# Kernel optimization log

Measured on AMD Instinct MI355X. Metric: run time of the kernel, lower is better.

## Reference

```python
import jax, jax.numpy as jnp
import numpy as np

EPS = 1e-5
HEADS = 8


def _bn(x, p):
    # p: [4, C] rows = (gamma, beta, running_mean, running_var); channel axis = 1 (eval-mode BN)
    shape = (1, p.shape[1]) + (1,) * (x.ndim - 2)
    g = p[0].reshape(shape); b = p[1].reshape(shape)
    m = p[2].reshape(shape); v = p[3].reshape(shape)
    return (x - m) * (g / jnp.sqrt(v + EPS)) + b


def _conv1x1(x, w):
    # x: [N, Cin, H, W], w: [Cout, Cin]
    return jnp.einsum('oc,nchw->nohw', w, x)


def _axial(x, kqv_w, kqv_bn, logits_bn, rel_enc, ks, height_dim):
    # x: [B, C, H, W]
    if height_dim:
        x = jnp.transpose(x, (0, 3, 1, 2))  # [B, W, C, H] -> attend over H (=ks)
    else:
        x = jnp.transpose(x, (0, 2, 1, 3))  # [B, H, C, W] -> attend over W (=ks)
    b, w, d, h = x.shape
    dh = d // HEADS
    xf = x.reshape(b * w, d, h)
    kqv = jnp.einsum('oc,ncl->nol', kqv_w, xf)          # conv1d k=1, [n, 2d, h]
    kqv = _bn(kqv, kqv_bn)
    kqv = kqv.reshape(b * w, HEADS, dh * 2, h)
    k = kqv[:, :, : dh // 2]                            # [n, H, dh/2, h]
    q = kqv[:, :, dh // 2: dh]                          # [n, H, dh/2, h]
    v = kqv[:, :, dh:]                                  # [n, H, dh,   h]
    # relative position encodings
    idx = jnp.arange(ks)[None, :] - jnp.arange(ks)[:, None] + ks - 1  # [ks, ks]
    rel = rel_enc[:, idx.reshape(-1)].reshape(dh * 2, ks, ks)
    q_enc = rel[: dh // 2]
    k_enc = rel[dh // 2: dh]
    v_enc = rel[dh:]
    qk = jnp.einsum('nhdx,nhdy->nhxy', q, k)
    qr = jnp.einsum('nhdx,dxy->nhxy', q, q_enc)
    kr = jnp.einsum('nhdx,dxy->nhyx', k, k_enc)         # einsum + transpose(2,3)
    logits = jnp.concatenate([qk, qr, kr], axis=1)       # [n, 3*H, h, h]
    logits = _bn(logits, logits_bn)
    logits = logits.reshape(b * w, 3, HEADS, h, h).sum(axis=1)
    weights = jax.nn.softmax(logits, axis=3)             # [n, H, h, h]
    attn = jnp.einsum('nhxy,nhdy->nhdx', weights, v)
    attn_enc = jnp.einsum('nhxy,dxy->nhdx', weights, v_enc)
    # cat along last dim + reshape + sum(dim=-2) in torch == elementwise sum here
    out = (attn + attn_enc).reshape(b, w, d, h)
    if height_dim:
        out = jnp.transpose(out, (0, 2, 3, 1))  # [B, C, H, W]
    else:
        out = jnp.transpose(out, (0, 2, 1, 3))  # [B, C, H, W]
    return out


def setup_inputs() -> dict:
    key = jax.random.key(0)
    ks = jax.random.split(key, 13)
    def rn(k, shape, s=0.05):
        return jax.random.normal(k, shape, jnp.float32) * s
    def rp(k, shape):
        return jax.random.uniform(k, shape, jnp.float32, minval=0.1, maxval=1.0)
    return {
        'x': jax.random.normal(ks[0], (1, 64, 256, 128), jnp.float32),
        'conv1_w': rn(ks[1], (64, 64)),
        'bn1': rp(ks[2], (4, 64)),
        'kqv_w_h': rn(ks[3], (128, 64)),
        'kqv_bn_h': rp(ks[4], (4, 128)),
        'logits_bn_h': rp(ks[5], (4, 24)),
        'rel_enc_h': rn(ks[6], (16, 511)),
        'kqv_w_w': rn(ks[7], (128, 64)),
        'kqv_bn_w': rp(ks[8], (4, 128)),
        'logits_bn_w': rp(ks[9], (4, 24)),
        'rel_enc_w': rn(ks[10], (16, 255)),
        'conv3_w': rn(ks[11], (64, 64)),
        'bn3': rp(ks[12], (4, 64)),
    }


def reference(x, conv1_w, bn1, kqv_w_h, kqv_bn_h, logits_bn_h, rel_enc_h,
              kqv_w_w, kqv_bn_w, logits_bn_w, rel_enc_w, conv3_w, bn3):
    out = jax.nn.relu(_bn(_conv1x1(x, conv1_w), bn1))
    out = _axial(out, kqv_w_h, kqv_bn_h, logits_bn_h, rel_enc_h, 256, True)
    out = _axial(out, kqv_w_w, kqv_bn_w, logits_bn_w, rel_enc_w, 128, False)
    out = jax.nn.relu(out)
    out = _bn(_conv1x1(out, conv3_w), bn3)
    return jax.nn.relu(out + x)
```

## Files before the change

kernel.cpp:

```cpp
#include <hip/hip_runtime.h>
#include <stdint.h>

#define EPSF 1e-5f
#define LOG2E 1.4426950408889634f

typedef float f32x2 __attribute__((ext_vector_type(2)));
typedef float f32x4 __attribute__((ext_vector_type(4)));

__device__ __forceinline__ float bflo(uint32_t u){ union{uint32_t u;float f;}c; c.u=u<<16; return c.f; }
__device__ __forceinline__ float bfhi(uint32_t u){ union{uint32_t u;float f;}c; c.u=u&0xffff0000u; return c.f; }
__device__ __forceinline__ float bfhiraw(uint32_t u){ union{uint32_t u;float f;}c; c.u=u; return c.f; }
__device__ __forceinline__ uint32_t f2bf(float f){ union{float f;uint32_t u;}c; c.f=f; uint32_t u=c.u; return (u + 0x7fffu + ((u>>16)&1u)) >> 16; }
__device__ __forceinline__ uint32_t pk2(float a, float b){ return f2bf(a) | (f2bf(b)<<16); }

__device__ __forceinline__ f32x2 pk_add(f32x2 a, f32x2 b){
  f32x2 d; asm("v_pk_add_f32 %0, %1, %2" : "=v"(d) : "v"(a), "v"(b)); return d;
}
__device__ __forceinline__ f32x2 pk_mul(f32x2 a, f32x2 b){
  f32x2 d; asm("v_pk_mul_f32 %0, %1, %2" : "=v"(d) : "v"(a), "v"(b)); return d;
}
__device__ __forceinline__ f32x2 pk_fma(f32x2 a, f32x2 b, f32x2 c){
  f32x2 d; asm("v_pk_fma_f32 %0, %1, %2, %3" : "=v"(d) : "v"(a), "v"(b), "v"(c)); return d;
}
__device__ __forceinline__ f32x2 up2(uint32_t u){
  f32x2 r; r.x = bflo(u); r.y = bfhiraw(u); return r;
}

__global__ void k_relpack(const float* __restrict__ relH, const float* __restrict__ relW,
                          uint4* __restrict__ rqkH, uint4* __restrict__ rveH,
                          uint4* __restrict__ rqkW, uint4* __restrict__ rveW) {
  int NJ = blockIdx.x ? 255 : 511;
  const float* rel = blockIdx.x ? relW : relH;
  uint4* rqk = blockIdx.x ? rqkW : rqkH;
  uint4* rve = blockIdx.x ? rveW : rveH;
  int j = threadIdx.x;
  if (j >= NJ) return;
  const float* q = rel;
  const float* k = rel + 4*NJ;
  const float* v = rel + 8*NJ;
  int jr = NJ-1-j;
  uint4 a;
  a.x = pk2(q[0*NJ+j], q[1*NJ+j]);
  a.y = pk2(q[2*NJ+j], q[3*NJ+j]);
  a.z = pk2(k[0*NJ+jr], k[1*NJ+jr]);
  a.w = pk2(k[2*NJ+jr], k[3*NJ+jr]);
  rqk[j] = a;
  uint4 b;
  b.x = pk2(v[0*NJ+j], v[1*NJ+j]);
  b.y = pk2(v[2*NJ+j], v[3*NJ+j]);
  b.z = pk2(v[4*NJ+j], v[5*NJ+j]);
  b.w = pk2(v[6*NJ+j], v[7*NJ+j]);
  rve[j] = b;
}

__global__ __launch_bounds__(256)
void k_conv1(const float* __restrict__ in, const float* __restrict__ w,
             const float* __restrict__ bn, float* __restrict__ out) {
  __shared__ float L[64*65];
  int tid = threadIdx.x;
  int p0 = blockIdx.x * 64;
  int lane = tid & 63;
  int wvs = __builtin_amdgcn_readfirstlane(tid >> 6);
  #pragma unroll
  for (int rr = 0; rr < 16; ++rr) {
    int c = wvs*16 + rr;
    L[lane*65 + c] = in[(size_t)c*32768 + p0 + lane];
  }
  __syncthreads();
  f32x2 xv2[32];
  #pragma unroll
  for (int c2 = 0; c2 < 32; ++c2) {
    xv2[c2].x = L[lane*65 + 2*c2];
    xv2[c2].y = L[lane*65 + 2*c2 + 1];
  }
  float val[16];
  #pragma unroll
  for (int r = 0; r < 16; ++r) {
    int o = wvs*16 + r;
    const f32x2* wr = (const f32x2*)(w + o*64);
    f32x2 a2 = {0.f, 0.f};
    #pragma unroll
    for (int c2 = 0; c2 < 32; ++c2) a2 = wr[c2]*xv2[c2] + a2;
    float acc = a2.x + a2.y;
    float s = bn[o] * rsqrtf(bn[192+o] + EPSF);
    val[r] = fmaxf(fmaf(acc, s, fmaf(-bn[128+o], s, bn[64+o])), 0.f);
  }
  __syncthreads();
  #pragma unroll
  for (int r = 0; r < 16; ++r) L[lane*65 + wvs*16 + r] = val[r];
  __syncthreads();
  float4* dst = (float4*)(out + (size_t)p0*64);
  #pragma unroll
  for (int k = 0; k < 4; ++k) {
    int f4 = tid + k*256;
    int f = f4*4; int p = f >> 6, o = f & 63;
    float4 v;
    v.x = L[p*65+o]; v.y = L[p*65+o+1]; v.z = L[p*65+o+2]; v.w = L[p*65+o+3];
    dst[f4] = v;
  }
}

template<int LEN, int RS, int CS>
__global__ __launch_bounds__(512)
void k_kqv(const float* __restrict__ in, const float* __restrict__ w,
           const float* __restrict__ bn, uint4* __restrict__ kvV,
           uint2* __restrict__ kvK, float* __restrict__ qb) {
  __shared__ float L[64*65];
  int tid = threadIdx.x;
  int n = blockIdx.x;
  int y0 = blockIdx.y * 64;
  #pragma unroll
  for (int rr = 0; rr < 8; ++rr) {
    int idx = tid + rr*512;
    int yy = idx >> 6, c = idx & 63;
    L[yy*65 + c] = in[((size_t)(y0+yy)*RS + (size_t)n*CS)*64 + c];
  }
  __syncthreads();
  int hd = __builtin_amdgcn_readfirstlane(tid >> 6);
  int yy = tid & 63;
  f32x2 xv2[32];
  #pragma unroll
  for (int c2 = 0; c2 < 32; ++c2) {
    xv2[c2].x = L[yy*65 + 2*c2];
    xv2[c2].y = L[yy*65 + 2*c2 + 1];
  }
  float val[16];
  #pragma unroll
  for (int r = 0; r < 16; ++r) {
    int o = hd*16 + r;
    const f32x2* wr = (const f32x2*)(w + o*64);
    f32x2 a2 = {0.f, 0.f};
    #pragma unroll
    for (int c2 = 0; c2 < 32; ++c2) a2 = wr[c2]*xv2[c2] + a2;
    float acc = a2.x + a2.y;
    float s = bn[o] * rsqrtf(bn[384+o] + EPSF);
    val[r] = fmaf(acc, s, fmaf(-bn[256+o], s, bn[128+o]));
  }
  size_t base = ((size_t)n*8 + hd)*LEN + (y0 + yy);
  kvK[base] = make_uint2(pk2(val[0],val[1]), pk2(val[2],val[3]));
  kvV[base] = make_uint4(pk2(val[8],val[9]),  pk2(val[10],val[11]),
                         pk2(val[12],val[13]), pk2(val[14],val[15]));
  float4 qq; qq.x = val[4]; qq.y = val[5]; qq.z = val[6]; qq.w = val[7];
  *(float4*)(qb + base*4) = qq;
}

struct E4 { f32x2 qe0, qe1, ke0, ke1; };
struct V4 { f32x2 a, b, c, d; };

__device__ __forceinline__ E4 upQK(uint4 u){
  E4 r; r.qe0 = up2(u.x); r.qe1 = up2(u.y); r.ke0 = up2(u.z); r.ke1 = up2(u.w); return r;
}
__device__ __forceinline__ V4 upVE(uint4 u){
  V4 r; r.a = up2(u.x); r.b = up2(u.y); r.c = up2(u.z); r.d = up2(u.w); return r;
}
__device__ __forceinline__ float pairA(f32x2 q01, f32x2 q23, const E4& e,
                                       f32x2 ktlo, f32x2 kthi) {
  f32x2 t0 = pk_add(q01, e.ke0);
  f32x2 t1 = pk_add(q23, e.ke1);
  f32x2 s  = pk_mul(t0, ktlo);
  s = pk_fma(t1, kthi, s);
  s = pk_fma(q01, e.qe0, s);
  s = pk_fma(q23, e.qe1, s);
  return s.x + s.y;
}
__device__ __forceinline__ void pairB(float ex, const V4& ve,
                                      f32x2 va01, f32x2 va23, f32x2 vb01, f32x2 vb23,
                                      f32x2* A, float& ss) {
  ss += ex;
  f32x2 e2; e2.x = ex; e2.y = ex;
  A[0] = pk_fma(e2, pk_add(va01, ve.a), A[0]);
  A[1] = pk_fma(e2, pk_add(va23, ve.b), A[1]);
  A[2] = pk_fma(e2, pk_add(vb01, ve.c), A[2]);
  A[3] = pk_fma(e2, pk_add(vb23, ve.d), A[3]);
}

template<int LEN, int G, bool RELUO, int XS, int NS>
__global__ __launch_bounds__(LEN/4*G, 2)
void k_attn5(const uint4* __restrict__ kvV, const uint2* __restrict__ kvK,
             const float* __restrict__ qb, const uint4* __restrict__ rqk,
             const uint4* __restrict__ rve, const float* __restrict__ lbn,
             float* __restrict__ out) {
  constexpr int NJ = 2*LEN-1;
  constexpr int NJ4 = (NJ+1)/4;
  constexpr int XT = LEN/4;
  constexpr int T = XT*G;
  constexpr int YR = LEN/G;
  constexpr size_t S1 = (size_t)LEN*48 + (size_t)NJ4*4*16*2;
  constexpr size_t S2 = (size_t)(G-1)*LEN*40;
  constexpr size_t PS = S1 > S2 ? S1 : S2;
  int n  = blockIdx.x >> 3;
  int hd = blockIdx.x & 7;
  int t  = threadIdx.x;

  __shared__ __align__(16) char pool[PS];
  f32x4* sKt = (f32x4*)(pool);
  f32x4* sVa = (f32x4*)(pool + (size_t)LEN*16);
  f32x4* sVb = (f32x4*)(pool + (size_t)LEN*32);
  uint4* tQK = (uint4*)(pool + (size_t)LEN*48);
  uint4* tVE = (uint4*)(pool + (size_t)LEN*48 + (size_t)NJ4*64);

  float A0L, A1L, A2L;
  {
    int c0 = hd, c1 = 8+hd, c2 = 16+hd;
    A0L = lbn[c0]*rsqrtf(lbn[72+c0]+EPSF)*LOG2E;
    A1L = lbn[c1]*rsqrtf(lbn[72+c1]+EPSF)*LOG2E;
    A2L = lbn[c2]*rsqrtf(lbn[72+c2]+EPSF)*LOG2E;
  }
  float A0g = (fabsf(A0L) > 1e-25f) ? A0L : copysignf(1e-25f, A0L);
  float ratio = A2L / A0g;

  size_t kvbase = ((size_t)n*8 + hd)*LEN;
  for (int i = t; i < LEN; i += T) {
    uint2 kk = kvK[kvbase + i];
    uint4 vv = kvV[kvbase + i];
    f32x4 kt; kt.x=bflo(kk.x)*A0g; kt.y=bfhi(kk.x)*A0g; kt.z=bflo(kk.y)*A0g; kt.w=bfhi(kk.y)*A0g;
    sKt[i] = kt;
    f32x4 va; va.x=bflo(vv.x); va.y=bfhi(vv.x); va.z=bflo(vv.y); va.w=bfhi(vv.y);
    sVa[i] = va;
    f32x4 vb; vb.x=bflo(vv.z); vb.y=bfhi(vv.z); vb.z=bflo(vv.w); vb.w=bfhi(vv.w);
    sVb[i] = vb;
  }
  for (int j = t; j < NJ; j += T) {
    uint4 a = rqk[j];
    uint4 sq;
    sq.x = pk2(bflo(a.x)*A1L,   bfhi(a.x)*A1L);
    sq.y = pk2(bflo(a.y)*A1L,   bfhi(a.y)*A1L);
    sq.z = pk2(bflo(a.z)*ratio, bfhi(a.z)*ratio);
    sq.w = pk2(bflo(a.w)*ratio, bfhi(a.w)*ratio);
    int r = j & 3, mm = j >> 2;
    tQK[r*NJ4 + mm] = sq;
    tVE[r*NJ4 + mm] = rve[j];
  }

  int g  = t / XT;
  int tl = t % XT;
  int y0 = g * YR;
  int x0 = 4 * tl;

  f32x2 q01[4], q23[4];
  #pragma unroll
  for (int i = 0; i < 4; ++i) {
    f32x4 qq = *(const f32x4*)(qb + (kvbase + x0 + i)*4);
    q01[i].x = qq.x; q01[i].y = qq.y;
    q23[i].x = qq.z; q23[i].y = qq.w;
  }

  float m[4], ss[4];
  f32x2 acc[4][4];
  #pragma unroll
  for (int i=0;i<4;++i){ m[i]=-3.0e38f; ss[i]=0.f;
    #pragma unroll
    for(int d=0;d<4;++d){ acc[i][d].x=0.f; acc[i][d].y=0.f; } }

  __syncthreads();

  int mi = ((y0 + LEN-1) >> 2) - tl;
  E4 Wq0 = upQK(tQK[0*NJ4 + mi]), Wq1 = upQK(tQK[1*NJ4 + mi]), Wq2 = upQK(tQK[2*NJ4 + mi]);
  V4 Wv0 = upVE(tVE[0*NJ4 + mi]), Wv1 = upVE(tVE[1*NJ4 + mi]), Wv2 = upVE(tVE[2*NJ4 + mi]);

  for (int cc = 0; cc < YR/4; ++cc) {
    int yb = y0 + 4*cc;
    int ma = mi + cc;
    int mb = ma + 1;
    float lr[4][4];
    E4 E3 = upQK(tQK[3*NJ4 + ma]);
    { f32x4 kt = sKt[yb]; f32x2 kl = kt.lo, kh = kt.hi;
      lr[0][0]=pairA(q01[0],q23[0],E3, kl,kh); lr[1][0]=pairA(q01[1],q23[1],Wq2,kl,kh);
      lr[2][0]=pairA(q01[2],q23[2],Wq1,kl,kh); lr[3][0]=pairA(q01[3],q23[3],Wq0,kl,kh); }
    E4 E0 = upQK(tQK[0*NJ4 + mb]);
    { f32x4 kt = sKt[yb+1]; f32x2 kl = kt.lo, kh = kt.hi;
      lr[0][1]=pairA(q01[0],q23[0],E0, kl,kh); lr[1][1]=pairA(q01[1],q23[1],E3, kl,kh);
      lr[2][1]=pairA(q01[2],q23[2],Wq2,kl,kh); lr[3][1]=pairA(q01[3],q23[3],Wq1,kl,kh); }
    E4 E1 = upQK(tQK[1*NJ4 + mb]);
    { f32x4 kt = sKt[yb+2]; f32x2 kl = kt.lo, kh = kt.hi;
      lr[0][2]=pairA(q01[0],q23[0],E1, kl,kh); lr[1][2]=pairA(q01[1],q23[1],E0, kl,kh);
      lr[2][2]=pairA(q01[2],q23[2],E3, kl,kh); lr[3][2]=pairA(q01[3],q23[3],Wq2,kl,kh); }
    E4 E2 = upQK(tQK[2*NJ4 + mb]);
    { f32x4 kt = sKt[yb+3]; f32x2 kl = kt.lo, kh = kt.hi;
      lr[0][3]=pairA(q01[0],q23[0],E2, kl,kh); lr[1][3]=pairA(q01[1],q23[1],E1, kl,kh);
      lr[2][3]=pairA(q01[2],q23[2],E0, kl,kh); lr[3][3]=pairA(q01[3],q23[3],E3, kl,kh); }
    Wq0 = E0; Wq1 = E1; Wq2 = E2;
    #pragma unroll
    for (int i = 0; i < 4; ++i) {
      float cm = fmaxf(fmaxf(lr[i][0], lr[i][1]), fmaxf(lr[i][2], lr[i][3]));
      float mn = fmaxf(m[i], cm);
      float sc = __builtin_amdgcn_exp2f(m[i] - mn);
      m[i] = mn; ss[i] *= sc;
      f32x2 sc2; sc2.x = sc; sc2.y = sc;
      #pragma unroll
      for (int d = 0; d < 4; ++d) acc[i][d] = pk_mul(acc[i][d], sc2);
    }
    V4 F3 = upVE(tVE[3*NJ4 + ma]);
    { f32x4 va = sVa[yb], vb = sVb[yb];
      pairB(__builtin_amdgcn_exp2f(lr[0][0]-m[0]), F3,  va.lo,va.hi,vb.lo,vb.hi, acc[0], ss[0]);
      pairB(__builtin_amdgcn_exp2f(lr[1][0]-m[1]), Wv2, va.lo,va.hi,vb.lo,vb.hi, acc[1], ss[1]);
      pairB(__builtin_amdgcn_exp2f(lr[2][0]-m[2]), Wv1, va.lo,va.hi,vb.lo,vb.hi, acc[2], ss[2]);
      pairB(__builtin_amdgcn_exp2f(lr[3][0]-m[3]), Wv0, va.lo,va.hi,vb.lo,vb.hi, acc[3], ss[3]); }
    V4 F0 = upVE(tVE[0*NJ4 + mb]);
    { f32x4 va = sVa[yb+1], vb = sVb[yb+1];
      pairB(__builtin_amdgcn_exp2f(lr[0][1]-m[0]), F0,  va.lo,va.hi,vb.lo,vb.hi, acc[0], ss[0]);
      pairB(__builtin_amdgcn_exp2f(lr[1][1]-m[1]), F3,  va.lo,va.hi,vb.lo,vb.hi, acc[1], ss[1]);
      pairB(__builtin_amdgcn_exp2f(lr[2][1]-m[2]), Wv2, va.lo,va.hi,vb.lo,vb.hi, acc[2], ss[2]);
      pairB(__builtin_amdgcn_exp2f(lr[3][1]-m[3]), Wv1, va.lo,va.hi,vb.lo,vb.hi, acc[3], ss[3]); }
    V4 F1 = upVE(tVE[1*NJ4 + mb]);
    { f32x4 va = sVa[yb+2], vb = sVb[yb+2];
      pairB(__builtin_amdgcn_exp2f(lr[0][2]-m[0]), F1,  va.lo,va.hi,vb.lo,vb.hi, acc[0], ss[0]);
      pairB(__builtin_amdgcn_exp2f(lr[1][2]-m[1]), F0,  va.lo,va.hi,vb.lo,vb.hi, acc[1], ss[1]);
      pairB(__builtin_amdgcn_exp2f(lr[2][2]-m[2]), F3,  va.lo,va.hi,vb.lo,vb.hi, acc[2], ss[2]);
      pairB(__builtin_amdgcn_exp2f(lr[3][2]-m[3]), Wv2, va.lo,va.hi,vb.lo,vb.hi, acc[3], ss[3]); }
    V4 F2 = upVE(tVE[2*NJ4 + mb]);
    { f32x4 va = sVa[yb+3], vb = sVb[yb+3];
      pairB(__builtin_amdgcn_exp2f(lr[0][3]-m[0]), F2,  va.lo,va.hi,vb.lo,vb.hi, acc[0], ss[0]);
      pairB(__builtin_amdgcn_exp2f(lr[1][3]-m[1]), F1,  va.lo,va.hi,vb.lo,vb.hi, acc[1], ss[1]);
      pairB(__builtin_amdgcn_exp2f(lr[2][3]-m[2]), F0,  va.lo,va.hi,vb.lo,vb.hi, acc[2], ss[2]);
      pairB(__builtin_amdgcn_exp2f(lr[3][3]-m[3]), F3,  va.lo,va.hi,vb.lo,vb.hi, acc[3], ss[3]); }
    Wv0 = F0; Wv1 = F1; Wv2 = F2;
  }

  __syncthreads();
  float4* M0 = (float4*)(pool);
  float4* M1 = (float4*)(pool + (size_t)(G-1)*LEN*16);
  float2* MS = (float2*)(pool + (size_t)(G-1)*LEN*32);
  if (g > 0) {
    #pragma unroll
    for (int i = 0; i < 4; ++i) {
      int slot = (g-1)*LEN + x0 + i;
      M0[slot] = make_float4(acc[i][0].x,acc[i][0].y,acc[i][1].x,acc[i][1].y);
      M1[slot] = make_float4(acc[i][2].x,acc[i][2].y,acc[i][3].x,acc[i][3].y);
      MS[slot] = make_float2(m[i], ss[i]);
    }
  }
  __syncthreads();
  if (g == 0) {
    #pragma unroll
    for (int i = 0; i < 4; ++i) {
      float M = m[i];
      float2 oms[G-1];
      #pragma unroll
      for (int gg = 1; gg < G; ++gg) {
        oms[gg-1] = MS[(gg-1)*LEN + x0 + i];
        M = fmaxf(M, oms[gg-1].x);
      }
      float w0 = __builtin_amdgcn_exp2f(m[i] - M);
      float st = ss[i]*w0;
      float a[8];
      a[0]=acc[i][0].x*w0; a[1]=acc[i][0].y*w0; a[2]=acc[i][1].x*w0; a[3]=acc[i][1].y*w0;
      a[4]=acc[i][2].x*w0; a[5]=acc[i][2].y*w0; a[6]=acc[i][3].x*w0; a[7]=acc[i][3].y*w0;
      #pragma unroll
      for (int gg = 1; gg < G; ++gg) {
        int slot = (gg-1)*LEN + x0 + i;
        float wg = __builtin_amdgcn_exp2f(oms[gg-1].x - M);
        st += oms[gg-1].y*wg;
        float4 a0 = M0[slot];
        float4 a1 = M1[slot];
        a[0] = fmaf(a0.x, wg, a[0]); a[1] = fmaf(a0.y, wg, a[1]);
        a[2] = fmaf(a0.z, wg, a[2]); a[3] = fmaf(a0.w, wg, a[3]);
        a[4] = fmaf(a1.x, wg, a[4]); a[5] = fmaf(a1.y, wg, a[5]);
        a[6] = fmaf(a1.z, wg, a[6]); a[7] = fmaf(a1.w, wg, a[7]);
      }
      float inv = 1.0f / st;
      float* dst = out + ((size_t)(x0+i)*XS + (size_t)n*NS)*64 + hd*8;
      float4 lo, hi;
      lo.x = a[0]*inv; lo.y = a[1]*inv; lo.z = a[2]*inv; lo.w = a[3]*inv;
      hi.x = a[4]*inv; hi.y = a[5]*inv; hi.z = a[6]*inv; hi.w = a[7]*inv;
      if (RELUO) {
        lo.x=fmaxf(lo.x,0.f); lo.y=fmaxf(lo.y,0.f); lo.z=fmaxf(lo.z,0.f); lo.w=fmaxf(lo.w,0.f);
        hi.x=fmaxf(hi.x,0.f); hi.y=fmaxf(hi.y,0.f); hi.z=fmaxf(hi.z,0.f); hi.w=fmaxf(hi.w,0.f);
      }
      *(float4*)dst = lo;
      *((float4*)dst + 1) = hi;
    }
  }
}

__global__ __launch_bounds__(256)
void k_conv3(const float* __restrict__ in, const float* __restrict__ w,
             const float* __restrict__ bn, const float* __restrict__ resid,
             float* __restrict__ out) {
  __shared__ float L[64*65];
  int tid = threadIdx.x;
  int p0 = blockIdx.x * 64;
  const float4* src = (const float4*)(in + (size_t)p0*64);
  #pragma unroll
  for (int k = 0; k < 4; ++k) {
    int f4 = tid + k*256;
    float4 v = src[f4];
    int f = f4*4; int p = f >> 6, o = f & 63;
    L[p*65+o] = v.x; L[p*65+o+1] = v.y; L[p*65+o+2] = v.z; L[p*65+o+3] = v.w;
  }
  __syncthreads();
  int lane = tid & 63;
  int wvs = __builtin_amdgcn_readfirstlane(tid >> 6);
  f32x2 xv2[32];
  #pragma unroll
  for (int c2 = 0; c2 < 32; ++c2) {
    xv2[c2].x = L[lane*65 + 2*c2];
    xv2[c2].y = L[lane*65 + 2*c2 + 1];
  }
  #pragma unroll
  for (int r = 0; r < 16; ++r) {
    int o = wvs*16 + r;
    const f32x2* wr = (const f32x2*)(w + o*64);
    f32x2 a2 = {0.f, 0.f};
    #pragma unroll
    for (int c2 = 0; c2 < 32; ++c2) a2 = wr[c2]*xv2[c2] + a2;
    float acc = a2.x + a2.y;
    float s = bn[o] * rsqrtf(bn[192+o] + EPSF);
    float val = fmaf(acc, s, fmaf(-bn[128+o], s, bn[64+o]));
    size_t idx = (size_t)o*32768 + p0 + lane;
    out[idx] = fmaxf(val + resid[idx], 0.f);
  }
}

extern "C" void kernel_launch(void* const* d_in, const int* in_sizes, int n_in,
                              void* d_out, int out_size, void* d_ws, size_t ws_size,
                              hipStream_t stream) {
  const float* x         = (const float*)d_in[0];
  const float* conv1_w   = (const float*)d_in[1];
  const float* bn1       = (const float*)d_in[2];
  const float* kqv_w_h   = (const float*)d_in[3];
  const float* kqv_bn_h  = (const float*)d_in[4];
  const float* lbn_h     = (const float*)d_in[5];
  const float* rel_h     = (const float*)d_in[6];
  const float* kqv_w_w   = (const float*)d_in[7];
  const float* kqv_bn_w  = (const float*)d_in[8];
  const float* lbn_w     = (const float*)d_in[9];
  const float* rel_w     = (const float*)d_in[10];
  const float* conv3_w   = (const float*)d_in[11];
  const float* bn3       = (const float*)d_in[12];
  float* outp = (float*)d_out;
  char* ws = (char*)d_ws;

  float* A    = (float*)(ws);
  uint4* kvV  = (uint4*)(ws + 8388608);
  uint2* kvK  = (uint2*)(ws + 12582912);
  float* qb   = (float*)(ws + 14680064);
  uint4* rqkH = (uint4*)(ws + 18874368);
  uint4* rveH = (uint4*)(ws + 18882560);
  uint4* rqkW = (uint4*)(ws + 18890752);
  uint4* rveW = (uint4*)(ws + 18894848);

  k_relpack<<<2, 512, 0, stream>>>(rel_h, rel_w, rqkH, rveH, rqkW, rveW);

  k_conv1<<<512, 256, 0, stream>>>(x, conv1_w, bn1, A);

  k_kqv<256,128,1><<<dim3(128,4), 512, 0, stream>>>(A, kqv_w_h, kqv_bn_h, kvV, kvK, qb);
  k_attn5<256,4,false,128,1><<<1024, 256, 0, stream>>>(kvV, kvK, qb, rqkH, rveH, lbn_h, A);

  k_kqv<128,1,128><<<dim3(256,2), 512, 0, stream>>>(A, kqv_w_w, kqv_bn_w, kvV, kvK, qb);
  k_attn5<128,4,true,1,128><<<2048, 128, 0, stream>>>(kvV, kvK, qb, rqkW, rveW, lbn_w, A);

  k_conv3<<<512, 256, 0, stream>>>(A, conv3_w, bn3, x, outp);
}
```

Before: 178.3 us.

## Split attention query rows across blocks and use more key groups with serial merge

The attention kernel gains a query-row tile parameter, so the height pass now splits each (n, head) into two blocks of 128 query rows, and both passes use 8 key groups instead of 4. The cross-group softmax merge becomes a sequential pairwise reduction through a small shared buffer sized for one group, with barriers per step. This is meant to raise the number of waves in flight and shorten each thread's key loop. In exchange, each block loads the full K/V and relative tables again, and the merge adds extra synchronisation rounds.

```diff
diff --git a/kernel.cpp b/kernel.cpp
--- a/kernel.cpp
+++ b/kernel.cpp
@@ -174,22 +174,26 @@
   A[3] = pk_fma(e2, pk_add(vb23, ve.d), A[3]);
 }
 
-template<int LEN, int G, bool RELUO, int XS, int NS>
-__global__ __launch_bounds__(LEN/4*G, 2)
-void k_attn5(const uint4* __restrict__ kvV, const uint2* __restrict__ kvK,
+template<int LEN, int XR, int G, bool RELUO, int XS, int NS>
+__global__ __launch_bounds__(XR/4*G, 2)
+void k_attn6(const uint4* __restrict__ kvV, const uint2* __restrict__ kvK,
              const float* __restrict__ qb, const uint4* __restrict__ rqk,
              const uint4* __restrict__ rve, const float* __restrict__ lbn,
              float* __restrict__ out) {
   constexpr int NJ = 2*LEN-1;
   constexpr int NJ4 = (NJ+1)/4;
-  constexpr int XT = LEN/4;
+  constexpr int XT = XR/4;
   constexpr int T = XT*G;
   constexpr int YR = LEN/G;
+  constexpr int NXB = LEN/XR;
   constexpr size_t S1 = (size_t)LEN*48 + (size_t)NJ4*4*16*2;
-  constexpr size_t S2 = (size_t)(G-1)*LEN*40;
+  constexpr size_t S2 = (size_t)XR*40;
   constexpr size_t PS = S1 > S2 ? S1 : S2;
-  int n  = blockIdx.x >> 3;
-  int hd = blockIdx.x & 7;
+  int bx = blockIdx.x;
+  int xh = bx % NXB;
+  int nh = bx / NXB;
+  int n  = nh >> 3;
+  int hd = nh & 7;
   int t  = threadIdx.x;
 
   __shared__ __align__(16) char pool[PS];
@@ -235,7 +239,7 @@
   int g  = t / XT;
   int tl = t % XT;
   int y0 = g * YR;
-  int x0 = 4 * tl;
+  int x0 = xh*XR + 4*tl;
 
   f32x2 q01[4], q23[4];
   #pragma unroll
@@ -254,7 +258,7 @@
 
   __syncthreads();
 
-  int mi = ((y0 + LEN-1) >> 2) - tl;
+  int mi = ((y0 + LEN-1) >> 2) - (x0 >> 2);
   E4 Wq0 = upQK(tQK[0*NJ4 + mi]), Wq1 = upQK(tQK[1*NJ4 + mi]), Wq2 = upQK(tQK[2*NJ4 + mi]);
   V4 Wv0 = upVE(tVE[0*NJ4 + mi]), Wv1 = upVE(tVE[1*NJ4 + mi]), Wv2 = upVE(tVE[2*NJ4 + mi]);
 
@@ -319,50 +323,54 @@
 
   __syncthreads();
   float4* M0 = (float4*)(pool);
-  float4* M1 = (float4*)(pool + (size_t)(G-1)*LEN*16);
-  float2* MS = (float2*)(pool + (size_t)(G-1)*LEN*32);
-  if (g > 0) {
+  float4* M1 = (float4*)(pool + (size_t)XR*16);
+  float2* MS = (float2*)(pool + (size_t)XR*32);
+  int xl = 4*tl;
+  for (int gg = 1; gg < G; ++gg) {
+    if (g == gg) {
+      #pragma unroll
+      for (int i = 0; i < 4; ++i) {
+        M0[xl+i] = make_float4(acc[i][0].x,acc[i][0].y,acc[i][1].x,acc[i][1].y);
+        M1[xl+i] = make_float4(acc[i][2].x,acc[i][2].y,acc[i][3].x,acc[i][3].y);
+        MS[xl+i] = make_float2(m[i], ss[i]);
+      }
+    }
+    __syncthreads();
+    if (g == 0) {
+      #pragma unroll
+      for (int i = 0; i < 4; ++i) {
+        float2 os = MS[xl+i];
+        float M = fmaxf(m[i], os.x);
+        float w0 = __builtin_amdgcn_exp2f(m[i] - M);
+        float wg = __builtin_amdgcn_exp2f(os.x - M);
+        m[i] = M;
+        ss[i] = ss[i]*w0 + os.y*wg;
+        float4 a0 = M0[xl+i];
+        float4 a1 = M1[xl+i];
+        f32x2 w02; w02.x=w0; w02.y=w0;
+        f32x2 wg2; wg2.x=wg; wg2.y=wg;
+        f32x2 b0; b0.x=a0.x; b0.y=a0.y;
+        f32x2 b1; b1.x=a0.z; b1.y=a0.w;
+        f32x2 b2; b2.x=a1.x; b2.y=a1.y;
+        f32x2 b3; b3.x=a1.z; b3.y=a1.w;
+        acc[i][0] = pk_fma(acc[i][0], w02, pk_mul(b0, wg2));
+        acc[i][1] = pk_fma(acc[i][1], w02, pk_mul(b1, wg2));
+        acc[i][2] = pk_fma(acc[i][2], w02, pk_mul(b2, wg2));
+        acc[i][3] = pk_fma(acc[i][3], w02, pk_mul(b3, wg2));
+      }
+    }
+    __syncthreads();
+  }
+  if (g == 0) {
     #pragma unroll
     for (int i = 0; i < 4; ++i) {
-      int slot = (g-1)*LEN + x0 + i;
-      M0[slot] = make_float4(acc[i][0].x,acc[i][0].y,acc[i][1].x,acc[i][1].y);
-      M1[slot] = make_float4(acc[i][2].x,acc[i][2].y,acc[i][3].x,acc[i][3].y);
-      MS[slot] = make_float2(m[i], ss[i]);
-    }
-  }
-  __syncthreads();
-  if (g == 0) {
-    #pragma unroll
-    for (int i = 0; i < 4; ++i) {
-      float M = m[i];
-      float2 oms[G-1];
-      #pragma unroll
-      for (int gg = 1; gg < G; ++gg) {
-        oms[gg-1] = MS[(gg-1)*LEN + x0 + i];
-        M = fmaxf(M, oms[gg-1].x);
-      }
-      float w0 = __builtin_amdgcn_exp2f(m[i] - M);
-      float st = ss[i]*w0;
-      float a[8];
-      a[0]=acc[i][0].x*w0; a[1]=acc[i][0].y*w0; a[2]=acc[i][1].x*w0; a[3]=acc[i][1].y*w0;
-      a[4]=acc[i][2].x*w0; a[5]=acc[i][2].y*w0; a[6]=acc[i][3].x*w0; a[7]=acc[i][3].y*w0;
-      #pragma unroll
-      for (int gg = 1; gg < G; ++gg) {
-        int slot = (gg-1)*LEN + x0 + i;
-        float wg = __builtin_amdgcn_exp2f(oms[gg-1].x - M);
-        st += oms[gg-1].y*wg;
-        float4 a0 = M0[slot];
-        float4 a1 = M1[slot];
-        a[0] = fmaf(a0.x, wg, a[0]); a[1] = fmaf(a0.y, wg, a[1]);
-        a[2] = fmaf(a0.z, wg, a[2]); a[3] = fmaf(a0.w, wg, a[3]);
-        a[4] = fmaf(a1.x, wg, a[4]); a[5] = fmaf(a1.y, wg, a[5]);
-        a[6] = fmaf(a1.z, wg, a[6]); a[7] = fmaf(a1.w, wg, a[7]);
-      }
-      float inv = 1.0f / st;
+      float inv = 1.0f / ss[i];
       float* dst = out + ((size_t)(x0+i)*XS + (size_t)n*NS)*64 + hd*8;
       float4 lo, hi;
-      lo.x = a[0]*inv; lo.y = a[1]*inv; lo.z = a[2]*inv; lo.w = a[3]*inv;
-      hi.x = a[4]*inv; hi.y = a[5]*inv; hi.z = a[6]*inv; hi.w = a[7]*inv;
+      lo.x = acc[i][0].x*inv; lo.y = acc[i][0].y*inv;
+      lo.z = acc[i][1].x*inv; lo.w = acc[i][1].y*inv;
+      hi.x = acc[i][2].x*inv; hi.y = acc[i][2].y*inv;
+      hi.z = acc[i][3].x*inv; hi.w = acc[i][3].y*inv;
       if (RELUO) {
         lo.x=fmaxf(lo.x,0.f); lo.y=fmaxf(lo.y,0.f); lo.z=fmaxf(lo.z,0.f); lo.w=fmaxf(lo.w,0.f);
         hi.x=fmaxf(hi.x,0.f); hi.y=fmaxf(hi.y,0.f); hi.z=fmaxf(hi.z,0.f); hi.w=fmaxf(hi.w,0.f);
@@ -445,10 +453,10 @@
   k_conv1<<<512, 256, 0, stream>>>(x, conv1_w, bn1, A);
 
   k_kqv<256,128,1><<<dim3(128,4), 512, 0, stream>>>(A, kqv_w_h, kqv_bn_h, kvV, kvK, qb);
-  k_attn5<256,4,false,128,1><<<1024, 256, 0, stream>>>(kvV, kvK, qb, rqkH, rveH, lbn_h, A);
+  k_attn6<256,128,8,false,128,1><<<2048, 256, 0, stream>>>(kvV, kvK, qb, rqkH, rveH, lbn_h, A);
 
   k_kqv<128,1,128><<<dim3(256,2), 512, 0, stream>>>(A, kqv_w_w, kqv_bn_w, kvV, kvK, qb);
-  k_attn5<128,4,true,1,128><<<2048, 128, 0, stream>>>(kvV, kvK, qb, rqkW, rveW, lbn_w, A);
+  k_attn6<128,128,8,true,1,128><<<2048, 256, 0, stream>>>(kvV, kvK, qb, rqkW, rveW, lbn_w, A);
 
   k_conv3<<<512, 256, 0, stream>>>(A, conv3_w, bn3, x, outp);
 }
```

After: 201.0 us. +12.7%, slower.
